# Optimization experiments

Hardware: AMD Instinct MI355X
Metric: run time of the kernel (lower is better)

## Reference

```python
import jax, jax.numpy as jnp
import numpy as np

D_MODEL = 1024
D_INNER = 2048
N_EXPERTS = 8
TOP_K = 2
INIT_STD = 0.02


def setup_inputs() -> dict:
    key = jax.random.key(0)
    ks = jax.random.split(key, 6)
    B, S = 2, 2048
    x = jax.random.normal(ks[0], (B, S, D_MODEL), dtype=jnp.float32)
    router_w = jax.random.normal(ks[1], (N_EXPERTS, D_MODEL), dtype=jnp.float32) * (INIT_STD * 0.1)
    router_b = jnp.zeros((N_EXPERTS,), dtype=jnp.float32)
    gate_w = jax.random.normal(ks[2], (N_EXPERTS, D_MODEL, D_INNER), dtype=jnp.float32) * INIT_STD
    up_w = jax.random.normal(ks[3], (N_EXPERTS, D_MODEL, D_INNER), dtype=jnp.float32) * INIT_STD
    down_w = jax.random.normal(ks[4], (N_EXPERTS, D_INNER, D_MODEL), dtype=jnp.float32) * INIT_STD
    return {"x": x, "router_w": router_w, "router_b": router_b,
            "gate_w": gate_w, "up_w": up_w, "down_w": down_w}


def reference(x, router_w, router_b, gate_w, up_w, down_w):
    # Router: softmax over experts, top-k, renormalize top-k probs.
    logits = jnp.einsum('bsd,ed->bse', x, router_w) + router_b          # [B,S,E]
    probs = jax.nn.softmax(logits, axis=-1)
    top_p, top_i = jax.lax.top_k(probs, TOP_K)                           # [B,S,K]
    top_p = top_p / jnp.sum(top_p, axis=-1, keepdims=True)
    # Per-expert combine weight: c[b,s,e] = sum_k top_p[b,s,k] * [top_i[b,s,k]==e]
    onehot = jax.nn.one_hot(top_i, N_EXPERTS, dtype=x.dtype)             # [B,S,K,E]
    combine = jnp.einsum('bsk,bske->bse', top_p, onehot)                 # [B,S,E]
    # SwiGLU FFN for every expert (dense form of the masked dispatch),
    # zeroed/weighted by combine coefficients.
    g = jnp.einsum('bsd,edf->ebsf', x, gate_w)                           # [E,B,S,F]
    u = jnp.einsum('bsd,edf->ebsf', x, up_w)
    h = jax.nn.silu(g) * u
    y = jnp.einsum('ebsf,efd->ebsd', h, down_w)                          # [E,B,S,D]
    out = jnp.einsum('ebsd,bse->bsd', y, combine)
    return out
```

## Files before the change

kernel.cpp:

```cpp
#include <hip/hip_runtime.h>
#include <hip/hip_bf16.h>
#include <stdint.h>

#define D_MODEL 1024
#define D_INNER 2048
#define NEXP 8
#define TOPK 2
#define BM 128
#define MAXT 72

typedef float f32x4 __attribute__((ext_vector_type(4)));
typedef short bf16x8 __attribute__((ext_vector_type(8)));

#define MEMFENCE asm volatile("" ::: "memory")

__device__ __forceinline__ unsigned short f2b(float f) {
    union { float f; uint32_t u; } v; v.f = f;
    uint32_t u = v.u;
    return (unsigned short)((u + 0x7fffu + ((u >> 16) & 1u)) >> 16);
}

__device__ __forceinline__ void gl_lds16(const void* g, void* l) {
    __builtin_amdgcn_global_load_lds((const __attribute__((address_space(1))) void*)g,
                                     (__attribute__((address_space(3))) void*)l, 16, 0, 0);
}

__global__ __launch_bounds__(256) void cast_x_kernel(
    const float* __restrict__ in, unsigned short* __restrict__ out, int n8)
{
    int i = blockIdx.x * 256 + threadIdx.x;
    if (i >= n8) return;
    const float4* p = (const float4*)(in + (size_t)i * 8);
    float4 a = p[0], b = p[1];
    unsigned short o[8] = {f2b(a.x), f2b(a.y), f2b(a.z), f2b(a.w),
                           f2b(b.x), f2b(b.y), f2b(b.z), f2b(b.w)};
    *(uint4*)(out + (size_t)i * 8) = *(uint4*)o;
}

__global__ __launch_bounds__(256) void tcast3_kernel(
    const float* __restrict__ gw, const float* __restrict__ uw, const float* __restrict__ dw,
    unsigned short* __restrict__ gT, unsigned short* __restrict__ uT, unsigned short* __restrict__ dT)
{
    __shared__ unsigned short S[64][68];
    int which = blockIdx.z >> 3;
    int e = blockIdx.z & 7;
    const float* in; unsigned short* out; int K, N;
    if (which == 0)      { in = gw; out = gT; K = D_MODEL; N = D_INNER; }
    else if (which == 1) { in = uw; out = uT; K = D_MODEL; N = D_INNER; }
    else                 { in = dw; out = dT; K = D_INNER; N = D_MODEL; }
    int n0 = blockIdx.x * 64, k0 = blockIdx.y * 64;
    if (n0 >= N || k0 >= K) return;
    const float* ib = in + (size_t)e * K * N;
    unsigned short* ob = out + (size_t)e * N * K;
    int tid = threadIdx.x;
    int kk = tid >> 4, nn4 = (tid & 15) * 4;
#pragma unroll
    for (int j = 0; j < 4; j++) {
        int k = kk + 16 * j;
        float4 v = *(const float4*)&ib[(size_t)(k0 + k) * N + n0 + nn4];
        ushort4 s; s.x = f2b(v.x); s.y = f2b(v.y); s.z = f2b(v.z); s.w = f2b(v.w);
        *(ushort4*)&S[k][nn4] = s;
    }
    __syncthreads();
    int nn = tid >> 4, kk4 = (tid & 15) * 4;
#pragma unroll
    for (int j = 0; j < 4; j++) {
        int n = nn + 16 * j;
        ushort4 s;
        s.x = S[kk4 + 0][n]; s.y = S[kk4 + 1][n];
        s.z = S[kk4 + 2][n]; s.w = S[kk4 + 3][n];
        *(ushort4*)&ob[(size_t)(n0 + n) * K + k0 + kk4] = s;
    }
}

__global__ __launch_bounds__(64) void router_kernel(
    const float* __restrict__ x, const float* __restrict__ rw,
    const float* __restrict__ rb, int* __restrict__ top_i,
    float* __restrict__ top_w, int T)
{
    int t = blockIdx.x;
    if (t >= T) return;
    int l = threadIdx.x;
    float xv[16];
#pragma unroll
    for (int i = 0; i < 16; i++) xv[i] = x[(size_t)t * D_MODEL + l + 64 * i];
    float logit[NEXP];
#pragma unroll
    for (int e = 0; e < NEXP; e++) {
        float acc = 0.f;
#pragma unroll
        for (int i = 0; i < 16; i++) acc += xv[i] * rw[e * D_MODEL + l + 64 * i];
#pragma unroll
        for (int s = 32; s > 0; s >>= 1) acc += __shfl_xor(acc, s, 64);
        logit[e] = acc + rb[e];
    }
    if (l == 0) {
        int i0 = 0; float m0 = logit[0];
#pragma unroll
        for (int e = 1; e < NEXP; e++) if (logit[e] > m0) { m0 = logit[e]; i0 = e; }
        int i1 = -1; float m1 = -3.0e38f;
#pragma unroll
        for (int e = 0; e < NEXP; e++) {
            if (e == i0) continue;
            if (logit[e] > m1) { m1 = logit[e]; i1 = e; }
        }
        float w0 = 1.f / (1.f + expf(m1 - m0));
        top_i[t * 2 + 0] = i0; top_i[t * 2 + 1] = i1;
        top_w[t * 2 + 0] = w0; top_w[t * 2 + 1] = 1.f - w0;
    }
}

__global__ __launch_bounds__(256) void bucket_kernel(
    const int* __restrict__ top_i, const float* __restrict__ top_w,
    int* __restrict__ meta, int* __restrict__ tok_of_slot,
    float* __restrict__ w_of_slot, int T)
{
    __shared__ int cnt[256][NEXP];
    __shared__ int pre[256][NEXP];
    __shared__ int tot[NEXP];
    __shared__ int off[NEXP + 1];
    int tid = threadIdx.x;
    int per = (T + 255) / 256;
    int t0 = tid * per;
    for (int e = 0; e < NEXP; e++) cnt[tid][e] = 0;
    for (int t = t0; t < t0 + per && t < T; t++)
        for (int k = 0; k < TOPK; k++) cnt[tid][top_i[t * 2 + k]]++;
    __syncthreads();
    if (tid < NEXP) {
        int run = 0;
        for (int i = 0; i < 256; i++) { pre[i][tid] = run; run += cnt[i][tid]; }
        tot[tid] = run;
    }
    __syncthreads();
    if (tid == 0) {
        off[0] = 0;
        for (int e = 0; e < NEXP; e++) off[e + 1] = off[e] + tot[e];
        for (int e = 0; e <= NEXP; e++) meta[e] = off[e];
        int nt = 0;
        for (int e = 0; e < NEXP; e++)
            for (int r = off[e]; r < off[e + 1]; r += BM)
                meta[16 + nt++] = (e << 16) | r;
        for (; nt < MAXT; nt++) meta[16 + nt] = -1;
    }
    __syncthreads();
    int lc[NEXP];
#pragma unroll
    for (int e = 0; e < NEXP; e++) lc[e] = 0;
    for (int t = t0; t < t0 + per && t < T; t++) {
        for (int k = 0; k < TOPK; k++) {
            int e = top_i[t * 2 + k];
            int slot = off[e] + pre[tid][e] + lc[e]++;
            tok_of_slot[slot] = t;
            w_of_slot[slot] = top_w[t * 2 + k];
        }
    }
}

__global__ __launch_bounds__(256, 2) void moe_gate_up(
    const unsigned short* __restrict__ xb, const unsigned short* __restrict__ wgT,
    const unsigned short* __restrict__ wuT, const int* __restrict__ meta,
    const int* __restrict__ tok_of_slot, unsigned short* __restrict__ H)
{
    extern __shared__ __align__(16) unsigned short lds[];

    int lin = blockIdx.x;
    int strip = (lin & 7) * 2 + ((lin >> 3) & 1);
    int tix = lin >> 4;
    int packed = meta[16 + tix];
    if (packed < 0) return;
    int e = packed >> 16, row0 = packed & 0xffff;
    int Mloc = min(BM, meta[e + 1] - row0);
    int f0 = strip * 128;

    int tid = threadIdx.x, wv = tid >> 6, lane = tid & 63;

    const unsigned short* srcA[2];
    const unsigned short* srcG[2];
    const unsigned short* srcU[2];
#pragma unroll
    for (int j = 0; j < 2; j++) {
        int row = j * 64 + (tid >> 2);
        int p = tid & 3;
        int koffA = 8 * (p ^ ((row >> 1) & 3));
        int slot = row0 + ((row < Mloc) ? row : 0);
        srcA[j] = xb + (size_t)tok_of_slot[slot] * D_MODEL + koffA;
        size_t wb = (size_t)e * D_MODEL * D_INNER + (size_t)(f0 + row) * D_MODEL + koffA;
        srcG[j] = wgT + wb;
        srcU[j] = wuT + wb;
    }

    int wm = wv >> 1, wn = wv & 1;
    int lrow = lane & 15, kgrp = lane >> 4;
    int co = 8 * (kgrp ^ ((lrow >> 1) & 3));

    int arow[4], brow[4];
#pragma unroll
    for (int fm = 0; fm < 4; fm++) arow[fm] = (wm * 64 + fm * 16 + lrow) * 32;
#pragma unroll
    for (int fn = 0; fn < 4; fn++) brow[fn] = (wn * 64 + fn * 16 + lrow) * 32;

    f32x4 accg[4][4], accu[4][4];
#pragma unroll
    for (int i = 0; i < 4; i++)
#pragma unroll
        for (int j = 0; j < 4; j++) {
            accg[i][j] = (f32x4){0.f, 0.f, 0.f, 0.f};
            accu[i][j] = (f32x4){0.f, 0.f, 0.f, 0.f};
        }

    auto stage = [&](int u) {
        int kk = u * 32;
        unsigned short* base = lds + (u % 3) * 12288;
#pragma unroll
        for (int j = 0; j < 2; j++) {
            int d = (j * 256 + wv * 64) * 8;
            gl_lds16(srcA[j] + kk, base + d);
            gl_lds16(srcG[j] + kk, base + 4096 + d);
            gl_lds16(srcU[j] + kk, base + 8192 + d);
        }
    };

    bf16x8 a[4], bg[4], bu[4];
    auto load_frags = [&](int u) {
        const unsigned short* base = lds + (u % 3) * 12288;
#pragma unroll
        for (int fm = 0; fm < 4; fm++) a[fm] = *(const bf16x8*)(base + arow[fm] + co);
#pragma unroll
        for (int fn = 0; fn < 4; fn++) {
            bg[fn] = *(const bf16x8*)(base + 4096 + brow[fn] + co);
            bu[fn] = *(const bf16x8*)(base + 8192 + brow[fn] + co);
        }
    };

    const int NT = D_MODEL / 32;
    stage(0); stage(1);
    MEMFENCE;
    asm volatile("s_waitcnt vmcnt(6)" ::: "memory");
    __builtin_amdgcn_s_barrier();
    MEMFENCE;
    load_frags(0);

    for (int t = 0; t < NT; ++t) {
        __builtin_amdgcn_sched_barrier(0);
        __builtin_amdgcn_s_setprio(1);
#pragma unroll
        for (int fm = 0; fm < 4; fm++)
#pragma unroll
            for (int fn = 0; fn < 4; fn++) {
                accg[fm][fn] = __builtin_amdgcn_mfma_f32_16x16x32_bf16(a[fm], bg[fn], accg[fm][fn], 0, 0, 0);
                accu[fm][fn] = __builtin_amdgcn_mfma_f32_16x16x32_bf16(a[fm], bu[fn], accu[fm][fn], 0, 0, 0);
            }
        __builtin_amdgcn_s_setprio(0);
        __builtin_amdgcn_sched_barrier(0);

        if (t + 2 < NT) {
            stage(t + 2);
            asm volatile("s_waitcnt vmcnt(6)" ::: "memory");
        } else if (t + 1 < NT) {
            asm volatile("s_waitcnt vmcnt(0)" ::: "memory");
        }
        __builtin_amdgcn_s_barrier();
        MEMFENCE;
        if (t + 1 < NT) load_frags(t + 1);
    }

#pragma unroll
    for (int fm = 0; fm < 4; fm++)
#pragma unroll
        for (int fn = 0; fn < 4; fn++)
#pragma unroll
            for (int r = 0; r < 4; r++) {
                int m = wm * 64 + fm * 16 + kgrp * 4 + r;
                if (m < Mloc) {
                    int n = wn * 64 + fn * 16 + lrow;
                    float g = accg[fm][fn][r], u = accu[fm][fn][r];
                    float h = g / (1.f + __expf(-g)) * u;
                    H[(size_t)(row0 + m) * D_INNER + f0 + n] = f2b(h);
                }
            }
}

__global__ __launch_bounds__(256, 2) void moe_down(
    const unsigned short* __restrict__ H, const unsigned short* __restrict__ wdT,
    const int* __restrict__ meta, const int* __restrict__ tok_of_slot,
    const float* __restrict__ w_of_slot, float* __restrict__ out, int S2)
{
    __shared__ unsigned short lds[3 * 8192];
    __shared__ int toks[BM];
    __shared__ float wts[BM];

    int lin = blockIdx.x;
    int d0 = (lin & 7) * 128;
    int tix = lin >> 3;
    int packed = meta[16 + tix];
    if (packed < 0) return;
    int e = packed >> 16, row0 = packed & 0xffff;
    int Mloc = min(BM, meta[e + 1] - row0);

    int tid = threadIdx.x, wv = tid >> 6, lane = tid & 63;
    if (tid < BM) {
        bool v = tid < Mloc;
        toks[tid] = v ? tok_of_slot[row0 + tid] : 0;
        wts[tid] = v ? w_of_slot[row0 + tid] : 0.f;
    }

    const unsigned short* srcA[2];
    const unsigned short* srcB[2];
#pragma unroll
    for (int j = 0; j < 2; j++) {
        int row = j * 64 + (tid >> 2);
        int p = tid & 3;
        int koff = 8 * (p ^ ((row >> 1) & 3));
        int slot = min(row0 + row, S2 - 1);
        srcA[j] = H + (size_t)slot * D_INNER + koff;
        srcB[j] = wdT + (size_t)e * D_INNER * D_MODEL + (size_t)(d0 + row) * D_INNER + koff;
    }

    int wm = wv >> 1, wn = wv & 1;
    int lrow = lane & 15, kgrp = lane >> 4;
    int co = 8 * (kgrp ^ ((lrow >> 1) & 3));

    int arow[4], brow[4];
#pragma unroll
    for (int fm = 0; fm < 4; fm++) arow[fm] = (wm * 64 + fm * 16 + lrow) * 32;
#pragma unroll
    for (int fn = 0; fn < 4; fn++) brow[fn] = (wn * 64 + fn * 16 + lrow) * 32;

    f32x4 acc[4][4];
#pragma unroll
    for (int i = 0; i < 4; i++)
#pragma unroll
        for (int j = 0; j < 4; j++) acc[i][j] = (f32x4){0.f, 0.f, 0.f, 0.f};

    auto stage = [&](int u) {
        int kk = u * 32;
        unsigned short* base = lds + (u % 3) * 8192;
#pragma unroll
        for (int j = 0; j < 2; j++) {
            int d = (j * 256 + wv * 64) * 8;
            gl_lds16(srcA[j] + kk, base + d);
            gl_lds16(srcB[j] + kk, base + 4096 + d);
        }
    };

    bf16x8 a[4], b[4];
    auto load_frags = [&](int u) {
        const unsigned short* base = lds + (u % 3) * 8192;
#pragma unroll
        for (int fm = 0; fm < 4; fm++) a[fm] = *(const bf16x8*)(base + arow[fm] + co);
#pragma unroll
        for (int fn = 0; fn < 4; fn++) b[fn] = *(const bf16x8*)(base + 4096 + brow[fn] + co);
    };

    const int NT = D_INNER / 32;
    stage(0); stage(1);
    MEMFENCE;
    asm volatile("s_waitcnt vmcnt(4)" ::: "memory");
    __builtin_amdgcn_s_barrier();
    MEMFENCE;
    load_frags(0);

    for (int t = 0; t < NT; ++t) {
        __builtin_amdgcn_sched_barrier(0);
        __builtin_amdgcn_s_setprio(1);
#pragma unroll
        for (int fm = 0; fm < 4; fm++)
#pragma unroll
            for (int fn = 0; fn < 4; fn++)
                acc[fm][fn] = __builtin_amdgcn_mfma_f32_16x16x32_bf16(a[fm], b[fn], acc[fm][fn], 0, 0, 0);
        __builtin_amdgcn_s_setprio(0);
        __builtin_amdgcn_sched_barrier(0);

        if (t + 2 < NT) {
            stage(t + 2);
            asm volatile("s_waitcnt vmcnt(4)" ::: "memory");
        } else if (t + 1 < NT) {
            asm volatile("s_waitcnt vmcnt(0)" ::: "memory");
        }
        __builtin_amdgcn_s_barrier();
        MEMFENCE;
        if (t + 1 < NT) load_frags(t + 1);
    }

#pragma unroll
    for (int fm = 0; fm < 4; fm++)
#pragma unroll
        for (int fn = 0; fn < 4; fn++)
#pragma unroll
            for (int r = 0; r < 4; r++) {
                int m = wm * 64 + fm * 16 + kgrp * 4 + r;
                if (m < Mloc) {
                    int n = wn * 64 + fn * 16 + lrow;
                    atomicAdd(&out[(size_t)toks[m] * D_MODEL + d0 + n], wts[m] * acc[fm][fn][r]);
                }
            }
}

extern "C" void kernel_launch(void* const* d_in, const int* in_sizes, int n_in,
                              void* d_out, int out_size, void* d_ws, size_t ws_size,
                              hipStream_t stream) {
    const float* x  = (const float*)d_in[0];
    const float* rw = (const float*)d_in[1];
    const float* rb = (const float*)d_in[2];
    const float* gw = (const float*)d_in[3];
    const float* uw = (const float*)d_in[4];
    const float* dw = (const float*)d_in[5];
    float* out = (float*)d_out;

    int T = in_sizes[0] / D_MODEL;
    int S2 = 2 * T;

    char* ws = (char*)d_ws;
    size_t cur = 0;
    auto take = [&](size_t bytes) { char* p = ws + cur; cur = (cur + bytes + 255) & ~(size_t)255; return p; };
    int*   top_i = (int*)take((size_t)S2 * 4);
    float* top_w = (float*)take((size_t)S2 * 4);
    int*   meta  = (int*)take(1024);
    int*   tos   = (int*)take((size_t)S2 * 4);
    float* wos   = (float*)take((size_t)S2 * 4);
    unsigned short* xb  = (unsigned short*)take((size_t)T * D_MODEL * 2);
    unsigned short* wgT = (unsigned short*)take((size_t)NEXP * D_MODEL * D_INNER * 2);
    unsigned short* wuT = (unsigned short*)take((size_t)NEXP * D_MODEL * D_INNER * 2);
    unsigned short* wdT = (unsigned short*)take((size_t)NEXP * D_MODEL * D_INNER * 2);
    unsigned short* H   = (unsigned short*)take((size_t)S2 * D_INNER * 2);

    static const int GU_LDS = 3 * 12288 * 2;
    hipFuncSetAttribute((const void*)moe_gate_up,
                        hipFuncAttributeMaxDynamicSharedMemorySize, GU_LDS);

    hipMemsetAsync(d_out, 0, (size_t)out_size * sizeof(float), stream);

    int n8 = T * D_MODEL / 8;
    cast_x_kernel<<<(n8 + 255) / 256, 256, 0, stream>>>(x, xb, n8);
    tcast3_kernel<<<dim3(32, 32, 24), 256, 0, stream>>>(gw, uw, dw, wgT, wuT, wdT);

    router_kernel<<<T, 64, 0, stream>>>(x, rw, rb, top_i, top_w, T);
    bucket_kernel<<<1, 256, 0, stream>>>(top_i, top_w, meta, tos, wos, T);

    moe_gate_up<<<MAXT * 16, 256, GU_LDS, stream>>>(xb, wgT, wuT, meta, tos, H);
    moe_down<<<MAXT * 8, 256, 0, stream>>>(H, wdT, meta, tos, wos, out, S2);
}
```

Before: 266.7 us.

## Enlarge MoE GEMM tiles to 512 threads with BK=64 double buffering

After: 269.8 us. Within noise of the previous version (+1.2%).

```diff
diff --git a/kernel.cpp b/kernel.cpp
--- a/kernel.cpp
+++ b/kernel.cpp
@@ -6,8 +6,8 @@
 #define D_INNER 2048
 #define NEXP 8
 #define TOPK 2
-#define BM 128
-#define MAXT 72
+#define T256 40
+#define T128 72
 
 typedef float f32x4 __attribute__((ext_vector_type(4)));
 typedef short bf16x8 __attribute__((ext_vector_type(8)));
@@ -23,18 +23,6 @@
 __device__ __forceinline__ void gl_lds16(const void* g, void* l) {
     __builtin_amdgcn_global_load_lds((const __attribute__((address_space(1))) void*)g,
                                      (__attribute__((address_space(3))) void*)l, 16, 0, 0);
-}
-
-__global__ __launch_bounds__(256) void cast_x_kernel(
-    const float* __restrict__ in, unsigned short* __restrict__ out, int n8)
-{
-    int i = blockIdx.x * 256 + threadIdx.x;
-    if (i >= n8) return;
-    const float4* p = (const float4*)(in + (size_t)i * 8);
-    float4 a = p[0], b = p[1];
-    unsigned short o[8] = {f2b(a.x), f2b(a.y), f2b(a.z), f2b(a.w),
-                           f2b(b.x), f2b(b.y), f2b(b.z), f2b(b.w)};
-    *(uint4*)(out + (size_t)i * 8) = *(uint4*)o;
 }
 
 __global__ __launch_bounds__(256) void tcast3_kernel(
@@ -75,8 +63,8 @@
 
 __global__ __launch_bounds__(64) void router_kernel(
     const float* __restrict__ x, const float* __restrict__ rw,
-    const float* __restrict__ rb, int* __restrict__ top_i,
-    float* __restrict__ top_w, int T)
+    const float* __restrict__ rb, unsigned short* __restrict__ xb,
+    int* __restrict__ top_i, float* __restrict__ top_w, int T)
 {
     int t = blockIdx.x;
     if (t >= T) return;
@@ -84,6 +72,8 @@
     float xv[16];
 #pragma unroll
     for (int i = 0; i < 16; i++) xv[i] = x[(size_t)t * D_MODEL + l + 64 * i];
+#pragma unroll
+    for (int i = 0; i < 16; i++) xb[(size_t)t * D_MODEL + l + 64 * i] = f2b(xv[i]);
     float logit[NEXP];
 #pragma unroll
     for (int e = 0; e < NEXP; e++) {
@@ -138,9 +128,14 @@
         for (int e = 0; e <= NEXP; e++) meta[e] = off[e];
         int nt = 0;
         for (int e = 0; e < NEXP; e++)
-            for (int r = off[e]; r < off[e + 1]; r += BM)
+            for (int r = off[e]; r < off[e + 1]; r += 256)
                 meta[16 + nt++] = (e << 16) | r;
-        for (; nt < MAXT; nt++) meta[16 + nt] = -1;
+        for (; nt < T256; nt++) meta[16 + nt] = -1;
+        nt = 0;
+        for (int e = 0; e < NEXP; e++)
+            for (int r = off[e]; r < off[e + 1]; r += 128)
+                meta[64 + nt++] = (e << 16) | r;
+        for (; nt < T128; nt++) meta[64 + nt] = -1;
     }
     __syncthreads();
     int lc[NEXP];
@@ -156,7 +151,7 @@
     }
 }
 
-__global__ __launch_bounds__(256, 2) void moe_gate_up(
+__global__ __launch_bounds__(512, 2) void moe_gate_up(
     const unsigned short* __restrict__ xb, const unsigned short* __restrict__ wgT,
     const unsigned short* __restrict__ wuT, const int* __restrict__ meta,
     const int* __restrict__ tok_of_slot, unsigned short* __restrict__ H)
@@ -169,35 +164,39 @@
     int packed = meta[16 + tix];
     if (packed < 0) return;
     int e = packed >> 16, row0 = packed & 0xffff;
-    int Mloc = min(BM, meta[e + 1] - row0);
+    int Mloc = min(256, meta[e + 1] - row0);
     int f0 = strip * 128;
 
     int tid = threadIdx.x, wv = tid >> 6, lane = tid & 63;
-
-    const unsigned short* srcA[2];
+    int c = tid & 7, rr = tid >> 3;
+
+    const unsigned short* srcA[4];
     const unsigned short* srcG[2];
     const unsigned short* srcU[2];
 #pragma unroll
+    for (int j = 0; j < 4; j++) {
+        int row = j * 64 + rr;
+        int slot = row0 + ((row < Mloc) ? row : 0);
+        srcA[j] = xb + (size_t)tok_of_slot[slot] * D_MODEL + 8 * (c ^ (row & 7));
+    }
+#pragma unroll
     for (int j = 0; j < 2; j++) {
-        int row = j * 64 + (tid >> 2);
-        int p = tid & 3;
-        int koffA = 8 * (p ^ ((row >> 1) & 3));
-        int slot = row0 + ((row < Mloc) ? row : 0);
-        srcA[j] = xb + (size_t)tok_of_slot[slot] * D_MODEL + koffA;
-        size_t wb = (size_t)e * D_MODEL * D_INNER + (size_t)(f0 + row) * D_MODEL + koffA;
-        srcG[j] = wgT + wb;
-        srcU[j] = wuT + wb;
+        int row = j * 64 + rr;
+        size_t wb = (size_t)e * D_MODEL * D_INNER + (size_t)(f0 + row) * D_MODEL + 8 * (c ^ (row & 7));
+        srcG[j] = wgT + wb; srcU[j] = wuT + wb;
     }
 
     int wm = wv >> 1, wn = wv & 1;
     int lrow = lane & 15, kgrp = lane >> 4;
-    int co = 8 * (kgrp ^ ((lrow >> 1) & 3));
+    int sw = lrow & 7;
+    int co0 = 8 * (kgrp ^ sw);
+    int co1 = 8 * ((4 + kgrp) ^ sw);
 
     int arow[4], brow[4];
 #pragma unroll
-    for (int fm = 0; fm < 4; fm++) arow[fm] = (wm * 64 + fm * 16 + lrow) * 32;
-#pragma unroll
-    for (int fn = 0; fn < 4; fn++) brow[fn] = (wn * 64 + fn * 16 + lrow) * 32;
+    for (int i = 0; i < 4; i++) arow[i] = (wm * 64 + i * 16 + lrow) * 64;
+#pragma unroll
+    for (int i = 0; i < 4; i++) brow[i] = (wn * 64 + i * 16 + lrow) * 64;
 
     f32x4 accg[4][4], accu[4][4];
 #pragma unroll
@@ -209,39 +208,50 @@
         }
 
     auto stage = [&](int u) {
-        int kk = u * 32;
-        unsigned short* base = lds + (u % 3) * 12288;
+        int kk = u * 64;
+        unsigned short* base = lds + (u & 1) * 32768;
+#pragma unroll
+        for (int j = 0; j < 4; j++)
+            gl_lds16(srcA[j] + kk, base + (j * 512 + wv * 64) * 8);
 #pragma unroll
         for (int j = 0; j < 2; j++) {
-            int d = (j * 256 + wv * 64) * 8;
-            gl_lds16(srcA[j] + kk, base + d);
-            gl_lds16(srcG[j] + kk, base + 4096 + d);
-            gl_lds16(srcU[j] + kk, base + 8192 + d);
+            gl_lds16(srcG[j] + kk, base + 16384 + (j * 512 + wv * 64) * 8);
+            gl_lds16(srcU[j] + kk, base + 24576 + (j * 512 + wv * 64) * 8);
         }
     };
 
     bf16x8 a[4], bg[4], bu[4];
-    auto load_frags = [&](int u) {
-        const unsigned short* base = lds + (u % 3) * 12288;
-#pragma unroll
-        for (int fm = 0; fm < 4; fm++) a[fm] = *(const bf16x8*)(base + arow[fm] + co);
-#pragma unroll
-        for (int fn = 0; fn < 4; fn++) {
-            bg[fn] = *(const bf16x8*)(base + 4096 + brow[fn] + co);
-            bu[fn] = *(const bf16x8*)(base + 8192 + brow[fn] + co);
-        }
+    auto load_frags = [&](int u, int co) {
+        const unsigned short* base = lds + (u & 1) * 32768;
+#pragma unroll
+        for (int i = 0; i < 4; i++) a[i] = *(const bf16x8*)(base + arow[i] + co);
+#pragma unroll
+        for (int i = 0; i < 4; i++) bg[i] = *(const bf16x8*)(base + 16384 + brow[i] + co);
+#pragma unroll
+        for (int i = 0; i < 4; i++) bu[i] = *(const bf16x8*)(base + 24576 + brow[i] + co);
     };
 
-    const int NT = D_MODEL / 32;
-    stage(0); stage(1);
+    const int NT = D_MODEL / 64;
+    stage(0);
     MEMFENCE;
-    asm volatile("s_waitcnt vmcnt(6)" ::: "memory");
+    asm volatile("s_waitcnt vmcnt(0)" ::: "memory");
     __builtin_amdgcn_s_barrier();
     MEMFENCE;
-    load_frags(0);
+    load_frags(0, co0);
 
     for (int t = 0; t < NT; ++t) {
+        if (t + 1 < NT) stage(t + 1);
         __builtin_amdgcn_sched_barrier(0);
+        __builtin_amdgcn_s_setprio(1);
+#pragma unroll
+        for (int fm = 0; fm < 4; fm++)
+#pragma unroll
+            for (int fn = 0; fn < 4; fn++) {
+                accg[fm][fn] = __builtin_amdgcn_mfma_f32_16x16x32_bf16(a[fm], bg[fn], accg[fm][fn], 0, 0, 0);
+                accu[fm][fn] = __builtin_amdgcn_mfma_f32_16x16x32_bf16(a[fm], bu[fn], accu[fm][fn], 0, 0, 0);
+            }
+        __builtin_amdgcn_s_setprio(0);
+        load_frags(t, co1);
         __builtin_amdgcn_s_setprio(1);
 #pragma unroll
         for (int fm = 0; fm < 4; fm++)
@@ -252,16 +262,10 @@
             }
         __builtin_amdgcn_s_setprio(0);
         __builtin_amdgcn_sched_barrier(0);
-
-        if (t + 2 < NT) {
-            stage(t + 2);
-            asm volatile("s_waitcnt vmcnt(6)" ::: "memory");
-        } else if (t + 1 < NT) {
-            asm volatile("s_waitcnt vmcnt(0)" ::: "memory");
-        }
+        asm volatile("s_waitcnt vmcnt(0)" ::: "memory");
         __builtin_amdgcn_s_barrier();
         MEMFENCE;
-        if (t + 1 < NT) load_frags(t + 1);
+        if (t + 1 < NT) load_frags(t + 1, co0);
     }
 
 #pragma unroll
@@ -280,51 +284,56 @@
             }
 }
 
-__global__ __launch_bounds__(256, 2) void moe_down(
+__global__ __launch_bounds__(512, 2) void moe_down(
     const unsigned short* __restrict__ H, const unsigned short* __restrict__ wdT,
     const int* __restrict__ meta, const int* __restrict__ tok_of_slot,
     const float* __restrict__ w_of_slot, float* __restrict__ out, int S2)
 {
-    __shared__ unsigned short lds[3 * 8192];
-    __shared__ int toks[BM];
-    __shared__ float wts[BM];
+    extern __shared__ __align__(16) unsigned short lds[];
+    __shared__ int toks[128];
+    __shared__ float wts[128];
 
     int lin = blockIdx.x;
-    int d0 = (lin & 7) * 128;
-    int tix = lin >> 3;
-    int packed = meta[16 + tix];
+    int d0 = (lin & 3) * 256;
+    int tix = lin >> 2;
+    int packed = meta[64 + tix];
     if (packed < 0) return;
     int e = packed >> 16, row0 = packed & 0xffff;
-    int Mloc = min(BM, meta[e + 1] - row0);
+    int Mloc = min(128, meta[e + 1] - row0);
 
     int tid = threadIdx.x, wv = tid >> 6, lane = tid & 63;
-    if (tid < BM) {
+    if (tid < 128) {
         bool v = tid < Mloc;
         toks[tid] = v ? tok_of_slot[row0 + tid] : 0;
         wts[tid] = v ? w_of_slot[row0 + tid] : 0.f;
     }
+    int c = tid & 7, rr = tid >> 3;
 
     const unsigned short* srcA[2];
-    const unsigned short* srcB[2];
+    const unsigned short* srcB[4];
 #pragma unroll
     for (int j = 0; j < 2; j++) {
-        int row = j * 64 + (tid >> 2);
-        int p = tid & 3;
-        int koff = 8 * (p ^ ((row >> 1) & 3));
+        int row = j * 64 + rr;
         int slot = min(row0 + row, S2 - 1);
-        srcA[j] = H + (size_t)slot * D_INNER + koff;
-        srcB[j] = wdT + (size_t)e * D_INNER * D_MODEL + (size_t)(d0 + row) * D_INNER + koff;
-    }
-
-    int wm = wv >> 1, wn = wv & 1;
+        srcA[j] = H + (size_t)slot * D_INNER + 8 * (c ^ (row & 7));
+    }
+#pragma unroll
+    for (int j = 0; j < 4; j++) {
+        int row = j * 64 + rr;
+        srcB[j] = wdT + (size_t)e * D_INNER * D_MODEL + (size_t)(d0 + row) * D_INNER + 8 * (c ^ (row & 7));
+    }
+
+    int wm = wv >> 2, wn = wv & 3;
     int lrow = lane & 15, kgrp = lane >> 4;
-    int co = 8 * (kgrp ^ ((lrow >> 1) & 3));
+    int sw = lrow & 7;
+    int co0 = 8 * (kgrp ^ sw);
+    int co1 = 8 * ((4 + kgrp) ^ sw);
 
     int arow[4], brow[4];
 #pragma unroll
-    for (int fm = 0; fm < 4; fm++) arow[fm] = (wm * 64 + fm * 16 + lrow) * 32;
-#pragma unroll
-    for (int fn = 0; fn < 4; fn++) brow[fn] = (wn * 64 + fn * 16 + lrow) * 32;
+    for (int i = 0; i < 4; i++) arow[i] = (wm * 64 + i * 16 + lrow) * 64;
+#pragma unroll
+    for (int i = 0; i < 4; i++) brow[i] = 8192 + (wn * 64 + i * 16 + lrow) * 64;
 
     f32x4 acc[4][4];
 #pragma unroll
@@ -333,35 +342,44 @@
         for (int j = 0; j < 4; j++) acc[i][j] = (f32x4){0.f, 0.f, 0.f, 0.f};
 
     auto stage = [&](int u) {
-        int kk = u * 32;
-        unsigned short* base = lds + (u % 3) * 8192;
-#pragma unroll
-        for (int j = 0; j < 2; j++) {
-            int d = (j * 256 + wv * 64) * 8;
-            gl_lds16(srcA[j] + kk, base + d);
-            gl_lds16(srcB[j] + kk, base + 4096 + d);
-        }
+        int kk = u * 64;
+        unsigned short* base = lds + (u & 1) * 24576;
+#pragma unroll
+        for (int j = 0; j < 2; j++)
+            gl_lds16(srcA[j] + kk, base + (j * 512 + wv * 64) * 8);
+#pragma unroll
+        for (int j = 0; j < 4; j++)
+            gl_lds16(srcB[j] + kk, base + 8192 + (j * 512 + wv * 64) * 8);
     };
 
     bf16x8 a[4], b[4];
-    auto load_frags = [&](int u) {
-        const unsigned short* base = lds + (u % 3) * 8192;
-#pragma unroll
-        for (int fm = 0; fm < 4; fm++) a[fm] = *(const bf16x8*)(base + arow[fm] + co);
-#pragma unroll
-        for (int fn = 0; fn < 4; fn++) b[fn] = *(const bf16x8*)(base + 4096 + brow[fn] + co);
+    auto load_frags = [&](int u, int co) {
+        const unsigned short* base = lds + (u & 1) * 24576;
+#pragma unroll
+        for (int i = 0; i < 4; i++) a[i] = *(const bf16x8*)(base + arow[i] + co);
+#pragma unroll
+        for (int i = 0; i < 4; i++) b[i] = *(const bf16x8*)(base + brow[i] + co);
     };
 
-    const int NT = D_INNER / 32;
-    stage(0); stage(1);
+    const int NT = D_INNER / 64;
+    stage(0);
     MEMFENCE;
-    asm volatile("s_waitcnt vmcnt(4)" ::: "memory");
+    asm volatile("s_waitcnt vmcnt(0)" ::: "memory");
     __builtin_amdgcn_s_barrier();
     MEMFENCE;
-    load_frags(0);
+    load_frags(0, co0);
 
     for (int t = 0; t < NT; ++t) {
+        if (t + 1 < NT) stage(t + 1);
         __builtin_amdgcn_sched_barrier(0);
+        __builtin_amdgcn_s_setprio(1);
+#pragma unroll
+        for (int fm = 0; fm < 4; fm++)
+#pragma unroll
+            for (int fn = 0; fn < 4; fn++)
+                acc[fm][fn] = __builtin_amdgcn_mfma_f32_16x16x32_bf16(a[fm], b[fn], acc[fm][fn], 0, 0, 0);
+        __builtin_amdgcn_s_setprio(0);
+        load_frags(t, co1);
         __builtin_amdgcn_s_setprio(1);
 #pragma unroll
         for (int fm = 0; fm < 4; fm++)
@@ -370,16 +388,10 @@
                 acc[fm][fn] = __builtin_amdgcn_mfma_f32_16x16x32_bf16(a[fm], b[fn], acc[fm][fn], 0, 0, 0);
         __builtin_amdgcn_s_setprio(0);
         __builtin_amdgcn_sched_barrier(0);
-
-        if (t + 2 < NT) {
-            stage(t + 2);
-            asm volatile("s_waitcnt vmcnt(4)" ::: "memory");
-        } else if (t + 1 < NT) {
-            asm volatile("s_waitcnt vmcnt(0)" ::: "memory");
-        }
+        asm volatile("s_waitcnt vmcnt(0)" ::: "memory");
         __builtin_amdgcn_s_barrier();
         MEMFENCE;
-        if (t + 1 < NT) load_frags(t + 1);
+        if (t + 1 < NT) load_frags(t + 1, co0);
     }
 
 #pragma unroll
@@ -424,19 +436,19 @@
     unsigned short* wdT = (unsigned short*)take((size_t)NEXP * D_MODEL * D_INNER * 2);
     unsigned short* H   = (unsigned short*)take((size_t)S2 * D_INNER * 2);
 
-    static const int GU_LDS = 3 * 12288 * 2;
+    static const int GU_LDS = 2 * 32768 * 2;
+    static const int DN_LDS = 2 * 24576 * 2;
     hipFuncSetAttribute((const void*)moe_gate_up,
                         hipFuncAttributeMaxDynamicSharedMemorySize, GU_LDS);
+    hipFuncSetAttribute((const void*)moe_down,
+                        hipFuncAttributeMaxDynamicSharedMemorySize, DN_LDS);
 
     hipMemsetAsync(d_out, 0, (size_t)out_size * sizeof(float), stream);
 
-    int n8 = T * D_MODEL / 8;
-    cast_x_kernel<<<(n8 + 255) / 256, 256, 0, stream>>>(x, xb, n8);
     tcast3_kernel<<<dim3(32, 32, 24), 256, 0, stream>>>(gw, uw, dw, wgT, wuT, wdT);
-
-    router_kernel<<<T, 64, 0, stream>>>(x, rw, rb, top_i, top_w, T);
+    router_kernel<<<T, 64, 0, stream>>>(x, rw, rb, xb, top_i, top_w, T);
     bucket_kernel<<<1, 256, 0, stream>>>(top_i, top_w, meta, tos, wos, T);
 
-    moe_gate_up<<<MAXT * 16, 256, GU_LDS, stream>>>(xb, wgT, wuT, meta, tos, H);
-    moe_down<<<MAXT * 8, 256, 0, stream>>>(H, wdT, meta, tos, wos, out, S2);
-}
+    moe_gate_up<<<T256 * 16, 512, GU_LDS, stream>>>(xb, wgT, wuT, meta, tos, H);
+    moe_down<<<T128 * 4, 512, DN_LDS, stream>>>(H, wdT, meta, tos, wos, out, S2);
+}
```
